# Kernel optimization log

Hardware: AMD Instinct MI355X
Metric: run time of the kernel (lower is better)

Reference implementation:

```python
import jax, jax.numpy as jnp
import numpy as np

# db2 decomposition filters (pywt values); pytorch_wavelets reverses them and uses
# F.conv1d (cross-correlation), so we store the reversed filters.
_DEC_LO = np.array([-0.12940952255092145, 0.22414386804185735,
                    0.836516303737469, 0.48296291314469025])
_DEC_HI = np.array([-0.48296291314469025, 0.836516303737469,
                    -0.22414386804185735, 0.12940952255092145])
_H0 = jnp.asarray(_DEC_LO[::-1].copy(), dtype=jnp.float32)
_H1 = jnp.asarray(_DEC_HI[::-1].copy(), dtype=jnp.float32)


def _dwt_layer(x):
    """Vectorized equivalent of DWTLayer: db2 J=1 DWT along the channel axis at
    every (b,i,j) pixel, keeping first C//2 lo coeffs then first C//2 hi coeffs.
    pytorch_wavelets mode='zero' with L=4 and even C -> pad 2 each side, stride 2.
    x: [B, C, H, W] -> [B, C, H, W]
    """
    B, C, H, W = x.shape
    v = jnp.transpose(x, (0, 2, 3, 1)).reshape(B * H * W, 1, C)
    filt = jnp.stack([_H0, _H1])[:, None, :].astype(x.dtype)  # [2,1,4]
    out = jax.lax.conv_general_dilated(
        v, filt, window_strides=(2,), padding=((2, 2),),
        dimension_numbers=('NCH', 'OIH', 'NCH'))  # [BHW, 2, C//2 + 1]
    half = C // 2
    t = jnp.concatenate([out[:, 0, :half], out[:, 1, :half]], axis=-1)
    return jnp.transpose(t.reshape(B, H, W, C), (0, 3, 1, 2))


def setup_inputs() -> dict:
    key = jax.random.key(0)
    ks = jax.random.split(key, 7)
    B, C, H, W = 16, 360, 64, 64
    return {
        'x': jax.random.normal(ks[0], (B, C, H, W), dtype=jnp.float32),
        'conv_w': jax.random.normal(ks[1], (1, 1, 2, 7), dtype=jnp.float32) * 0.1,
        'conv_b': jax.random.normal(ks[2], (1,), dtype=jnp.float32) * 0.1,
        'w1': jax.random.normal(ks[3], (128, 90), dtype=jnp.float32) * 0.1,
        'b1': jax.random.normal(ks[4], (128,), dtype=jnp.float32) * 0.1,
        'w2': jax.random.normal(ks[5], (256, 128), dtype=jnp.float32) * 0.1,
        'b2': jax.random.normal(ks[6], (256,), dtype=jnp.float32) * 0.1,
    }


def reference(x, conv_w, conv_b, w1, b1, w2, b2):
    x = _dwt_layer(x)                     # [B,360,H,W]
    cd1 = x[:, 180:, :, :]                # detail half -> [B,180,H,W]
    cd1 = _dwt_layer(cd1)                 # [B,180,H,W]
    cd1 = cd1.reshape(-1, 1, 2, 90)       # torch .view(-1,2,90).unsqueeze(1)
    cd1 = jax.lax.conv_general_dilated(
        cd1, conv_w, window_strides=(1, 1), padding=((0, 0), (3, 3)),
        dimension_numbers=('NCHW', 'OIHW', 'NCHW'))
    cd1 = cd1 + conv_b[None, :, None, None]   # [N,1,1,90]
    cd1 = jax.nn.relu(cd1)
    cd1 = cd1.reshape(cd1.shape[0], 1, -1)    # [N,1,90]
    cd1 = jax.nn.relu(cd1 @ w1.T + b1)        # [N,1,128]
    out = cd1 @ w2.T + b2                     # [N,1,256]
    return out.reshape(-1, 256, 8, 8)
```

## Files before the change

### kernel.cpp

```cpp
#include <hip/hip_runtime.h>

using bf8   = __attribute__((ext_vector_type(8))) short;
using f32x4 = __attribute__((ext_vector_type(4))) float;

__device__ inline unsigned short f2bf(float f) {
  unsigned u = __float_as_uint(f);
  return (unsigned short)((u + 0x7FFFu + ((u >> 16) & 1u)) >> 16);
}
__device__ inline float bf2f(unsigned short h) {
  return __uint_as_float(((unsigned)h) << 16);
}

struct Gs { float g0[10]; float g1[10]; };
__host__ __device__ constexpr Gs make_g() {
  double H0[4] = {0.48296291314469025, 0.836516303737469,
                  0.22414386804185735, -0.12940952255092145};
  double H1[4] = {0.12940952255092145, -0.22414386804185735,
                  0.836516303737469, -0.48296291314469025};
  Gs r{};
  for (int d = 0; d < 10; ++d) {
    double a = 0.0, b = 0.0;
    for (int k = 0; k < 4; ++k) {
      int j = d - 2 * k;
      if (j >= 0 && j < 4) { a += H0[k] * H1[j]; b += H1[k] * H1[j]; }
    }
    r.g0[d] = (float)a; r.g1[d] = (float)b;
  }
  return r;
}

__global__ __launch_bounds__(256) void dwt2_kernel(const float* __restrict__ x,
                                                   unsigned short* __restrict__ A) {
  constexpr Gs G = make_g();
  const int bx    = blockIdx.x;
  const int seg   = bx & 3;
  const int pb    = bx >> 2;
  const int b     = pb >> 3;
  const int chunk = pb & 7;
  const int s     = chunk * 512 + 2 * threadIdx.x;

  const float2* xb = (const float2*)(x + (size_t)b * 360 * 4096 + s);
  unsigned short* Ab = A + (size_t)b * 180 * 4096 + s;

  const int c0 = (seg * 90) >> 2;
  const int c1 = ((seg + 1) * 90) >> 2;

  float2 w[10];
  const int base = 4 * c0 - 6;
#pragma unroll
  for (int i = 0; i < 10; ++i) {
    int idx = base + i;
    w[i] = (idx >= 0) ? xb[(size_t)idx * 2048] : float2{0.f, 0.f};
  }

  for (int c = c0; c < c1; ++c) {
    float2 nx[4];
    const bool pf = (c + 1 < c1);
    const int nb = 4 * c + 4;
#pragma unroll
    for (int i = 0; i < 4; ++i)
      nx[i] = pf ? xb[(size_t)(nb + i) * 2048] : float2{0.f, 0.f};

    float2 lo{0.f, 0.f}, hi{0.f, 0.f};
#pragma unroll
    for (int d = 0; d < 10; ++d) {
      lo.x = fmaf(G.g0[d], w[d].x, lo.x);
      lo.y = fmaf(G.g0[d], w[d].y, lo.y);
      hi.x = fmaf(G.g1[d], w[d].x, hi.x);
      hi.y = fmaf(G.g1[d], w[d].y, hi.y);
    }
    *(ushort2*)&Ab[(size_t)c * 4096]        = ushort2{f2bf(lo.x), f2bf(lo.y)};
    *(ushort2*)&Ab[(size_t)(c + 90) * 4096] = ushort2{f2bf(hi.x), f2bf(hi.y)};
#pragma unroll
    for (int i = 0; i < 6; ++i) w[i] = w[i + 4];
#pragma unroll
    for (int i = 0; i < 4; ++i) w[6 + i] = nx[i];
  }
}

__global__ __launch_bounds__(256) void conv_kernel(
    const unsigned short* __restrict__ A,
    const float* __restrict__ cw, const float* __restrict__ cb,
    unsigned short* __restrict__ Y) {
  __shared__ float As[64 * 180];
  const int tid = threadIdx.x;
  const size_t g0 = (size_t)blockIdx.x * 64;

  const uint4* src = (const uint4*)(A + g0 * 180);
  for (int i = tid; i < 1440; i += 256) {
    uint4 v = src[i];
    float* d = &As[8 * i];
    d[0] = bf2f((unsigned short)(v.x & 0xFFFF));
    d[1] = bf2f((unsigned short)(v.x >> 16));
    d[2] = bf2f((unsigned short)(v.y & 0xFFFF));
    d[3] = bf2f((unsigned short)(v.y >> 16));
    d[4] = bf2f((unsigned short)(v.z & 0xFFFF));
    d[5] = bf2f((unsigned short)(v.z >> 16));
    d[6] = bf2f((unsigned short)(v.w & 0xFFFF));
    d[7] = bf2f((unsigned short)(v.w >> 16));
  }
  __syncthreads();

  float cwr[14];
#pragma unroll
  for (int k = 0; k < 14; ++k) cwr[k] = cw[k];
  const float cbv = cb[0];

  for (int i = tid; i < 64 * 24; i += 256) {
    const int g = i / 24, j4 = i - g * 24, j0 = 4 * j4;
    const float* Ag = &As[g * 180];
    float v0[10], v1[10];
#pragma unroll
    for (int t = 0; t < 10; ++t) {
      const int m = j0 - 3 + t;
      const bool ok = (m >= 0) && (m < 90);
      v0[t] = ok ? Ag[m] : 0.0f;
      v1[t] = ok ? Ag[90 + m] : 0.0f;
    }
    ushort4 o4;
    unsigned short* op = (unsigned short*)&o4;
#pragma unroll
    for (int d = 0; d < 4; ++d) {
      const int j = j0 + d;
      float acc = 0.0f;
      if (j < 90) {
        acc = cbv;
#pragma unroll
        for (int k = 0; k < 7; ++k) {
          acc = fmaf(v0[d + k], cwr[k], acc);
          acc = fmaf(v1[d + k], cwr[7 + k], acc);
        }
        acc = fmaxf(acc, 0.0f);
      }
      op[d] = f2bf(acc);
    }
    *(ushort4*)&Y[(g0 + g) * 96 + j0] = o4;
  }
}

__global__ __launch_bounds__(512) void mlp_mfma_kernel(
    const unsigned short* __restrict__ Y,
    const float* __restrict__ w1, const float* __restrict__ b1,
    const float* __restrict__ w2, const float* __restrict__ b2,
    float* __restrict__ out) {
  __shared__ unsigned short w1B[128 * 104];
  __shared__ unsigned short w2B[256 * 136];
  __shared__ unsigned short HY[128 * 136];
  __shared__ float b1s[128];
  __shared__ float b2s[256];

  const int tid = threadIdx.x;
  const size_t g0 = (size_t)blockIdx.x * 128;

  for (int i = tid; i < 128 * 90; i += 512) {
    const int o = i / 90, k = i - o * 90;
    w1B[o * 104 + k] = f2bf(w1[i]);
  }
  for (int i = tid; i < 128 * 6; i += 512) {
    const int o = i / 6, k = 90 + (i - o * 6);
    w1B[o * 104 + k] = 0;
  }
  const float4* w2v = (const float4*)w2;
  for (int i = tid; i < 8192; i += 512) {
    const int o = i >> 5, k4 = i & 31;
    const float4 v = w2v[i];
    *(ushort4*)&w2B[o * 136 + 4 * k4] =
        ushort4{f2bf(v.x), f2bf(v.y), f2bf(v.z), f2bf(v.w)};
  }
  const uint4* ys = (const uint4*)(Y + g0 * 96);
  for (int i = tid; i < 1536; i += 512) {
    const int r = i / 12, c8 = i - r * 12;
    *(uint4*)&HY[r * 104 + 8 * c8] = ys[i];
  }
  if (tid < 128) b1s[tid] = b1[tid];
  if (tid < 256) b2s[tid] = b2[tid];
  __syncthreads();

  const int w = tid >> 6, lane = tid & 63;
  const int l15 = lane & 15, q = lane >> 4;
  const int mrow = 16 * w + l15;

  bf8 ya[3];
#pragma unroll
  for (int ks = 0; ks < 3; ++ks)
    ya[ks] = *(const bf8*)&HY[mrow * 104 + 32 * ks + 8 * q];

  f32x4 acc1[8];
#pragma unroll
  for (int nt = 0; nt < 8; ++nt) {
    f32x4 a = {0.f, 0.f, 0.f, 0.f};
#pragma unroll
    for (int ks = 0; ks < 3; ++ks) {
      const bf8 wb = *(const bf8*)&w1B[(16 * nt + l15) * 104 + 32 * ks + 8 * q];
      a = __builtin_amdgcn_mfma_f32_16x16x32_bf16(ya[ks], wb, a, 0, 0, 0);
    }
    acc1[nt] = a;
  }
  __syncthreads();

#pragma unroll
  for (int nt = 0; nt < 8; ++nt) {
#pragma unroll
    for (int r = 0; r < 4; ++r) {
      const int n = 16 * w + 4 * q + r;
      const int o = 16 * nt + l15;
      float v = acc1[nt][r] + b1s[o];
      v = fmaxf(v, 0.0f);
      HY[n * 136 + o] = f2bf(v);
    }
  }
  __syncthreads();

  bf8 ha[4];
#pragma unroll
  for (int ks = 0; ks < 4; ++ks)
    ha[ks] = *(const bf8*)&HY[mrow * 136 + 32 * ks + 8 * q];

#pragma unroll 4
  for (int nt = 0; nt < 16; ++nt) {
    f32x4 a = {0.f, 0.f, 0.f, 0.f};
#pragma unroll
    for (int ks = 0; ks < 4; ++ks) {
      const bf8 wb = *(const bf8*)&w2B[(16 * nt + l15) * 136 + 32 * ks + 8 * q];
      a = __builtin_amdgcn_mfma_f32_16x16x32_bf16(ha[ks], wb, a, 0, 0, 0);
    }
#pragma unroll
    for (int r = 0; r < 4; ++r) {
      const int n = 16 * w + 4 * q + r;
      const int o = 16 * nt + l15;
      out[(g0 + n) * 256 + o] = a[r] + b2s[o];
    }
  }
}

extern "C" void kernel_launch(void* const* d_in, const int* in_sizes, int n_in,
                              void* d_out, int out_size, void* d_ws, size_t ws_size,
                              hipStream_t stream) {
  const float* x  = (const float*)d_in[0];
  const float* cw = (const float*)d_in[1];
  const float* cb = (const float*)d_in[2];
  const float* w1 = (const float*)d_in[3];
  const float* b1 = (const float*)d_in[4];
  const float* w2 = (const float*)d_in[5];
  const float* b2 = (const float*)d_in[6];
  float* outp = (float*)d_out;

  unsigned short* Abf = (unsigned short*)d_ws;
  unsigned short* Ybf = Abf + (size_t)16 * 180 * 4096;

  dwt2_kernel<<<512, 256, 0, stream>>>(x, Abf);
  conv_kernel<<<1024, 256, 0, stream>>>(Abf, cw, cb, Ybf);
  mlp_mfma_kernel<<<512, 512, 0, stream>>>(Ybf, w1, b1, w2, b2, outp);
}
```

Before: 215.2 us.

## Precompute bf16 MLP weights in extra DWT blocks and split MLP output columns

Extra blocks appended to the DWT launch convert w1 and w2 to padded bf16 once in the workspace, so each MLP block copies ready-made weights instead of converting fp32 on every block. The MLP kernel becomes 256-thread blocks over 64 rows, each handling one half of the 256 output columns, which shrinks shared memory and quadruples the block count. The DWT kernel now processes four pixels per thread with float4 loads over 8 channel segments. The cost is recomputing the first layer twice per row group.

```diff
diff --git a/kernel.cpp b/kernel.cpp
--- a/kernel.cpp
+++ b/kernel.cpp
@@ -29,48 +29,73 @@
   return r;
 }
 
-__global__ __launch_bounds__(256) void dwt2_kernel(const float* __restrict__ x,
-                                                   unsigned short* __restrict__ A) {
+__global__ __launch_bounds__(256) void dwt2_kernel(
+    const float* __restrict__ x, unsigned short* __restrict__ A,
+    const float* __restrict__ w1, const float* __restrict__ w2,
+    unsigned short* __restrict__ w1b, unsigned short* __restrict__ w2b) {
+  const int bx = blockIdx.x;
+  if (bx >= 512) {
+    const int e = bx - 512;
+#pragma unroll
+    for (int t = 0; t < 4; ++t) {
+      const int i = e * 1024 + t * 256 + threadIdx.x;
+      if (i < 13312) {
+        const int o = i / 104, k = i - 104 * o;
+        w1b[i] = (k < 90) ? f2bf(w1[o * 90 + k]) : (unsigned short)0;
+      } else {
+        const int j = i - 13312;
+        const int o = j / 136, k = j - 136 * o;
+        w2b[j] = (k < 128) ? f2bf(w2[o * 128 + k]) : (unsigned short)0;
+      }
+    }
+    return;
+  }
+
   constexpr Gs G = make_g();
-  const int bx    = blockIdx.x;
-  const int seg   = bx & 3;
-  const int pb    = bx >> 2;
-  const int b     = pb >> 3;
-  const int chunk = pb & 7;
-  const int s     = chunk * 512 + 2 * threadIdx.x;
-
-  const float2* xb = (const float2*)(x + (size_t)b * 360 * 4096 + s);
+  const int seg   = bx & 7;
+  const int pb    = bx >> 3;
+  const int b     = pb >> 2;
+  const int chunk = pb & 3;
+  const int s     = chunk * 1024 + 4 * threadIdx.x;
+
+  const float4* xb = (const float4*)(x + (size_t)b * 360 * 4096 + s);
   unsigned short* Ab = A + (size_t)b * 180 * 4096 + s;
 
-  const int c0 = (seg * 90) >> 2;
-  const int c1 = ((seg + 1) * 90) >> 2;
-
-  float2 w[10];
+  const int c0 = (seg * 90) >> 3;
+  const int c1 = ((seg + 1) * 90) >> 3;
+
+  float4 w[10];
   const int base = 4 * c0 - 6;
 #pragma unroll
   for (int i = 0; i < 10; ++i) {
-    int idx = base + i;
-    w[i] = (idx >= 0) ? xb[(size_t)idx * 2048] : float2{0.f, 0.f};
+    const int idx = base + i;
+    w[i] = (idx >= 0) ? xb[(size_t)idx * 1024] : float4{0.f, 0.f, 0.f, 0.f};
   }
 
   for (int c = c0; c < c1; ++c) {
-    float2 nx[4];
+    float4 nx[4];
     const bool pf = (c + 1 < c1);
     const int nb = 4 * c + 4;
 #pragma unroll
     for (int i = 0; i < 4; ++i)
-      nx[i] = pf ? xb[(size_t)(nb + i) * 2048] : float2{0.f, 0.f};
-
-    float2 lo{0.f, 0.f}, hi{0.f, 0.f};
+      nx[i] = pf ? xb[(size_t)(nb + i) * 1024] : float4{0.f, 0.f, 0.f, 0.f};
+
+    float4 lo{0.f, 0.f, 0.f, 0.f}, hi{0.f, 0.f, 0.f, 0.f};
 #pragma unroll
     for (int d = 0; d < 10; ++d) {
       lo.x = fmaf(G.g0[d], w[d].x, lo.x);
       lo.y = fmaf(G.g0[d], w[d].y, lo.y);
+      lo.z = fmaf(G.g0[d], w[d].z, lo.z);
+      lo.w = fmaf(G.g0[d], w[d].w, lo.w);
       hi.x = fmaf(G.g1[d], w[d].x, hi.x);
       hi.y = fmaf(G.g1[d], w[d].y, hi.y);
-    }
-    *(ushort2*)&Ab[(size_t)c * 4096]        = ushort2{f2bf(lo.x), f2bf(lo.y)};
-    *(ushort2*)&Ab[(size_t)(c + 90) * 4096] = ushort2{f2bf(hi.x), f2bf(hi.y)};
+      hi.z = fmaf(G.g1[d], w[d].z, hi.z);
+      hi.w = fmaf(G.g1[d], w[d].w, hi.w);
+    }
+    *(ushort4*)&Ab[(size_t)c * 4096] =
+        ushort4{f2bf(lo.x), f2bf(lo.y), f2bf(lo.z), f2bf(lo.w)};
+    *(ushort4*)&Ab[(size_t)(c + 90) * 4096] =
+        ushort4{f2bf(hi.x), f2bf(hi.y), f2bf(hi.z), f2bf(hi.w)};
 #pragma unroll
     for (int i = 0; i < 6; ++i) w[i] = w[i + 4];
 #pragma unroll
@@ -138,42 +163,33 @@
   }
 }
 
-__global__ __launch_bounds__(512) void mlp_mfma_kernel(
+__global__ __launch_bounds__(256) void mlp_mfma_kernel(
     const unsigned short* __restrict__ Y,
-    const float* __restrict__ w1, const float* __restrict__ b1,
-    const float* __restrict__ w2, const float* __restrict__ b2,
+    const unsigned short* __restrict__ w1b,
+    const unsigned short* __restrict__ w2b,
+    const float* __restrict__ b1, const float* __restrict__ b2,
     float* __restrict__ out) {
   __shared__ unsigned short w1B[128 * 104];
-  __shared__ unsigned short w2B[256 * 136];
-  __shared__ unsigned short HY[128 * 136];
-  __shared__ float b1s[128];
-  __shared__ float b2s[256];
+  __shared__ unsigned short w2B[128 * 136];
+  __shared__ unsigned short HY[64 * 136];
+  __shared__ float bias[256];
 
   const int tid = threadIdx.x;
-  const size_t g0 = (size_t)blockIdx.x * 128;
-
-  for (int i = tid; i < 128 * 90; i += 512) {
-    const int o = i / 90, k = i - o * 90;
-    w1B[o * 104 + k] = f2bf(w1[i]);
-  }
-  for (int i = tid; i < 128 * 6; i += 512) {
-    const int o = i / 6, k = 90 + (i - o * 6);
-    w1B[o * 104 + k] = 0;
-  }
-  const float4* w2v = (const float4*)w2;
-  for (int i = tid; i < 8192; i += 512) {
-    const int o = i >> 5, k4 = i & 31;
-    const float4 v = w2v[i];
-    *(ushort4*)&w2B[o * 136 + 4 * k4] =
-        ushort4{f2bf(v.x), f2bf(v.y), f2bf(v.z), f2bf(v.w)};
-  }
-  const uint4* ys = (const uint4*)(Y + g0 * 96);
-  for (int i = tid; i < 1536; i += 512) {
-    const int r = i / 12, c8 = i - r * 12;
-    *(uint4*)&HY[r * 104 + 8 * c8] = ys[i];
-  }
-  if (tid < 128) b1s[tid] = b1[tid];
-  if (tid < 256) b2s[tid] = b2[tid];
+  const int fam = blockIdx.x & 1;
+  const size_t g0 = (size_t)(blockIdx.x >> 1) * 64;
+
+  {
+    const uint4* s1 = (const uint4*)w1b;
+    for (int i = tid; i < 1664; i += 256) ((uint4*)w1B)[i] = s1[i];
+    const uint4* s2 = (const uint4*)(w2b + (size_t)fam * 128 * 136);
+    for (int i = tid; i < 2176; i += 256) ((uint4*)w2B)[i] = s2[i];
+    const uint4* ys = (const uint4*)(Y + g0 * 96);
+    for (int i = tid; i < 768; i += 256) {
+      const int r = i / 12, c = i - 12 * r;
+      *(uint4*)&HY[r * 104 + 8 * c] = ys[i];
+    }
+    bias[tid] = (tid < 128) ? b1[tid] : b2[fam * 128 + (tid - 128)];
+  }
   __syncthreads();
 
   const int w = tid >> 6, lane = tid & 63;
@@ -204,9 +220,7 @@
     for (int r = 0; r < 4; ++r) {
       const int n = 16 * w + 4 * q + r;
       const int o = 16 * nt + l15;
-      float v = acc1[nt][r] + b1s[o];
-      v = fmaxf(v, 0.0f);
-      HY[n * 136 + o] = f2bf(v);
+      HY[n * 136 + o] = f2bf(fmaxf(acc1[nt][r] + bias[o], 0.0f));
     }
   }
   __syncthreads();
@@ -216,8 +230,8 @@
   for (int ks = 0; ks < 4; ++ks)
     ha[ks] = *(const bf8*)&HY[mrow * 136 + 32 * ks + 8 * q];
 
-#pragma unroll 4
-  for (int nt = 0; nt < 16; ++nt) {
+#pragma unroll 2
+  for (int nt = 0; nt < 8; ++nt) {
     f32x4 a = {0.f, 0.f, 0.f, 0.f};
 #pragma unroll
     for (int ks = 0; ks < 4; ++ks) {
@@ -228,7 +242,7 @@
     for (int r = 0; r < 4; ++r) {
       const int n = 16 * w + 4 * q + r;
       const int o = 16 * nt + l15;
-      out[(g0 + n) * 256 + o] = a[r] + b2s[o];
+      out[(g0 + n) * 256 + fam * 128 + o] = a[r] + bias[128 + o];
     }
   }
 }
@@ -247,8 +261,10 @@
 
   unsigned short* Abf = (unsigned short*)d_ws;
   unsigned short* Ybf = Abf + (size_t)16 * 180 * 4096;
-
-  dwt2_kernel<<<512, 256, 0, stream>>>(x, Abf);
+  unsigned short* w1b = Ybf + (size_t)65536 * 96;
+  unsigned short* w2b = w1b + 13312;
+
+  dwt2_kernel<<<559, 256, 0, stream>>>(x, Abf, w1, w2, w1b, w2b);
   conv_kernel<<<1024, 256, 0, stream>>>(Abf, cw, cb, Ybf);
-  mlp_mfma_kernel<<<512, 512, 0, stream>>>(Ybf, w1, b1, w2, b2, outp);
-}
+  mlp_mfma_kernel<<<2048, 256, 0, stream>>>(Ybf, w1b, w2b, b1, b2, outp);
+}
```

New measurement: 213.5 us. No clear change (-0.8%).
